# Kernel optimization log

Measured on AMD Instinct MI355X. Metric: run time of the kernel, lower is better.

Reference implementation:

```python
import jax, jax.numpy as jnp
import numpy as np

B = 8192
INPUT_DIM = 1024
HIDDEN = 4096
LATENT = 256
K = 16384  # codebook size
COMMIT = 0.25


def setup_inputs() -> dict:
    key = jax.random.key(0)
    ks = jax.random.split(key, 12)

    def lin(k, fan_in, fan_out):
        bound = 1.0 / np.sqrt(fan_in)
        kw, kb = jax.random.split(k)
        W = jax.random.uniform(kw, (fan_in, fan_out), jnp.float32, -bound, bound)
        b = jax.random.uniform(kb, (fan_out,), jnp.float32, -bound, bound)
        return W, b

    eW1, eb1 = lin(ks[0], INPUT_DIM, HIDDEN)
    eW2, eb2 = lin(ks[1], HIDDEN, HIDDEN)
    eW3, eb3 = lin(ks[2], HIDDEN, LATENT)
    dW1, db1 = lin(ks[3], LATENT, HIDDEN)
    dW2, db2 = lin(ks[4], HIDDEN, HIDDEN)
    dW3, db3 = lin(ks[5], HIDDEN, INPUT_DIM)
    codebook = jax.random.uniform(ks[6], (K, LATENT), jnp.float32, -1.0 / K, 1.0 / K)
    x = jax.random.normal(ks[7], (B, INPUT_DIM), jnp.float32)
    return {
        "x": x,
        "eW1": eW1, "eb1": eb1, "eW2": eW2, "eb2": eb2, "eW3": eW3, "eb3": eb3,
        "codebook": codebook,
        "dW1": dW1, "db1": db1, "dW2": dW2, "db2": db2, "dW3": dW3, "db3": db3,
    }


def _encoder(x, eW1, eb1, eW2, eb2, eW3, eb3):
    h = jax.nn.relu(x @ eW1 + eb1)          # dropout is identity in eval
    h = jax.nn.relu(h @ eW2 + eb2)
    return jnp.tanh(h @ eW3 + eb3)          # [B, LATENT]


def _decoder(z, dW1, db1, dW2, db2, dW3, db3):
    h = jax.nn.relu(z @ dW1 + db1)
    h = jax.nn.relu(h @ dW2 + db2)
    return h @ dW3 + db3                    # [B, INPUT_DIM]


def _vq(z, codebook):
    # pairwise squared distances: ||z||^2 + ||e||^2 - 2 z.e^T   -> [B, K]
    d = (jnp.sum(z * z, axis=1, keepdims=True)
         + jnp.sum(codebook * codebook, axis=1)
         - 2.0 * (z @ codebook.T))
    idx = jnp.argmin(d, axis=1)                              # [B]
    enc = jax.nn.one_hot(idx, K, dtype=jnp.float32)          # [B, K]
    q = enc @ codebook                                       # [B, LATENT]
    e_loss = jnp.mean((jax.lax.stop_gradient(q) - z) ** 2)
    q_loss = jnp.mean((q - jax.lax.stop_gradient(z)) ** 2)
    vq_loss = q_loss + COMMIT * e_loss
    q_st = z + jax.lax.stop_gradient(q - z)                  # straight-through
    avg_probs = jnp.mean(enc, axis=0)
    perplexity = jnp.exp(-jnp.sum(avg_probs * jnp.log(avg_probs + 1e-10)))
    return q_st, idx, vq_loss, perplexity


def reference(x, eW1, eb1, eW2, eb2, eW3, eb3, codebook,
              dW1, db1, dW2, db2, dW3, db3):
    z = _encoder(x, eW1, eb1, eW2, eb2, eW3, eb3)
    q, tokens, vq_loss, perplexity = _vq(z, codebook)
    recon = _decoder(q, dW1, db1, dW2, db2, dW3, db3)
    recon_loss = jnp.mean((recon - x) ** 2)
    total = vq_loss + recon_loss
    return recon, tokens, vq_loss, recon_loss, total, perplexity
```

## Files before the change

### kernel.cpp

```cpp
#include <hip/hip_runtime.h>
#include <stdint.h>

#define B_N 8192
#define D_IN 1024
#define D_HID 4096
#define D_LAT 256
#define K_CB 16384

typedef __attribute__((ext_vector_type(8))) short bf16x8;
typedef __attribute__((ext_vector_type(4))) float f32x4;

enum { EPI_RELU = 0, EPI_TANH = 1, EPI_RECON = 2, EPI_VQ = 3 };
enum { MEPI_RELU = 0, MEPI_RECON = 1 };

__device__ __forceinline__ unsigned short f2b(float v) {
  unsigned u = __float_as_uint(v);
  u += 0x7fffu + ((u >> 16) & 1u);
  return (unsigned short)(u >> 16);
}

template <int EPI, bool BT>
__global__ __launch_bounds__(256, 2) void gemm_k(
    const float* __restrict__ A, const float* __restrict__ Bm,
    const float* __restrict__ bias, float* __restrict__ C, int M, int N, int K,
    const float* __restrict__ zz, const float* __restrict__ ee,
    unsigned long long* __restrict__ keys, const float* __restrict__ xref,
    double* __restrict__ accums) {
  constexpr int BSTR = BT ? 132 : 128;
  __shared__ float As[16 * 260];
  __shared__ float Bs[16 * 132];
  const int tid = threadIdx.x;
  const int w = tid >> 6;
  const int tx = tid & 15, ty = tid >> 4;
  const int m0 = blockIdx.y << 8, n0 = blockIdx.x << 7;

  float acc[16][8];
#pragma unroll
  for (int i = 0; i < 16; ++i)
#pragma unroll
    for (int j = 0; j < 8; ++j) acc[i][j] = 0.0f;

  for (int k0 = 0; k0 < K; k0 += 16) {
#pragma unroll
    for (int r = 0; r < 4; ++r) {
      const int f = tid + (r << 8);
      const int m = f >> 2, kq = (f & 3) << 2;
      const float4 v = *(const float4*)(A + (size_t)(m0 + m) * K + k0 + kq);
      As[(kq + 0) * 260 + m] = v.x;
      As[(kq + 1) * 260 + m] = v.y;
      As[(kq + 2) * 260 + m] = v.z;
      As[(kq + 3) * 260 + m] = v.w;
    }
    if (!BT) {
#pragma unroll
      for (int r = 0; r < 2; ++r) {
        const int f = tid + (r << 8);
        const float* gp = Bm + (size_t)(k0 + (f >> 5)) * N + n0 + ((f & 31) << 2);
        __builtin_amdgcn_global_load_lds((const unsigned int*)gp,
                                         (unsigned int*)&Bs[(r << 10) + (w << 8)],
                                         16, 0, 0);
      }
    } else {
#pragma unroll
      for (int r = 0; r < 2; ++r) {
        const int f = tid + (r << 8);
        const int n = f >> 2, kq = (f & 3) << 2;
        const float4 v = *(const float4*)(Bm + (size_t)(n0 + n) * K + k0 + kq);
        Bs[(kq + 0) * BSTR + n] = v.x;
        Bs[(kq + 1) * BSTR + n] = v.y;
        Bs[(kq + 2) * BSTR + n] = v.z;
        Bs[(kq + 3) * BSTR + n] = v.w;
      }
    }
    __syncthreads();
#pragma unroll
    for (int kk = 0; kk < 16; ++kk) {
      float a[16], b[8];
#pragma unroll
      for (int q = 0; q < 4; ++q)
        *(float4*)(a + (q << 2)) = *(const float4*)(&As[kk * 260 + (q << 6) + (ty << 2)]);
      *(float4*)(b) = *(const float4*)(&Bs[kk * BSTR + (tx << 2)]);
      *(float4*)(b + 4) = *(const float4*)(&Bs[kk * BSTR + 64 + (tx << 2)]);
#pragma unroll
      for (int i = 0; i < 16; ++i)
#pragma unroll
        for (int j = 0; j < 8; ++j) acc[i][j] = fmaf(a[i], b[j], acc[i][j]);
    }
    __syncthreads();
  }

  if (EPI == EPI_VQ) {
    float zr[16];
#pragma unroll
    for (int i = 0; i < 16; ++i)
      zr[i] = zz[m0 + ((i >> 2) << 6) + (ty << 2) + (i & 3)];
    float ev[8];
    *(float4*)(ev) = *(const float4*)(ee + n0 + (tx << 2));
    *(float4*)(ev + 4) = *(const float4*)(ee + n0 + 64 + (tx << 2));
#pragma unroll
    for (int i = 0; i < 16; ++i) {
      unsigned long long bk = ~0ull;
#pragma unroll
      for (int j = 0; j < 8; ++j) {
        const int col = n0 + ((j >> 2) << 6) + (tx << 2) + (j & 3);
        const float t = zr[i] + ev[j];
        const float d = t - 2.0f * acc[i][j];
        unsigned u = __float_as_uint(d);
        u = (u & 0x80000000u) ? ~u : (u | 0x80000000u);
        const unsigned long long key = ((unsigned long long)u << 32) | (unsigned)col;
        bk = key < bk ? key : bk;
      }
#pragma unroll
      for (int s = 1; s <= 8; s <<= 1) {
        const unsigned long long o = __shfl_xor(bk, s);
        if (o < bk) bk = o;
      }
      if (tx == 0) {
        const int row = m0 + ((i >> 2) << 6) + (ty << 2) + (i & 3);
        atomicMin(keys + row, bk);
      }
    }
    return;
  }

  float bb[8];
  *(float4*)(bb) = *(const float4*)(bias + n0 + (tx << 2));
  *(float4*)(bb + 4) = *(const float4*)(bias + n0 + 64 + (tx << 2));
  double lsum = 0.0;
#pragma unroll
  for (int i = 0; i < 16; ++i) {
    const int row = m0 + ((i >> 2) << 6) + (ty << 2) + (i & 3);
    float vrow[8];
#pragma unroll
    for (int j = 0; j < 8; ++j) {
      float v = acc[i][j] + bb[j];
      if (EPI == EPI_RELU) v = fmaxf(v, 0.0f);
      if (EPI == EPI_TANH) v = tanhf(v);
      if (EPI == EPI_RECON) {
        const int col = n0 + ((j >> 2) << 6) + (tx << 2) + (j & 3);
        const float xr = xref[(size_t)row * N + col];
        const float df = v - xr;
        lsum += (double)df * (double)df;
      }
      vrow[j] = v;
    }
    *(float4*)(C + (size_t)row * N + n0 + (tx << 2)) = *(float4*)(vrow);
    *(float4*)(C + (size_t)row * N + n0 + 64 + (tx << 2)) = *(float4*)(vrow + 4);
  }
  if (EPI == EPI_RECON) {
#pragma unroll
    for (int o = 32; o; o >>= 1) lsum += __shfl_down(lsum, o);
    if ((tid & 63) == 0) atomicAdd(accums + 1, lsum);
  }
}

template <int EPI>
__global__ __launch_bounds__(256, 2) void gemm_s(
    const float* __restrict__ A, const float* __restrict__ Bm,
    const float* __restrict__ bias, float* __restrict__ C, int M, int N, int K) {
  __shared__ float As[16][128];
  __shared__ float Bs[16][128];
  const int tid = threadIdx.x;
  const int tx = tid & 15, ty = tid >> 4;
  const int m0 = blockIdx.y << 7, n0 = blockIdx.x << 7;
  float acc[8][8];
#pragma unroll
  for (int i = 0; i < 8; ++i)
#pragma unroll
    for (int j = 0; j < 8; ++j) acc[i][j] = 0.0f;
  for (int k0 = 0; k0 < K; k0 += 16) {
#pragma unroll
    for (int r = 0; r < 2; ++r) {
      const int f = tid + (r << 8);
      const int m = f >> 2, kq = (f & 3) << 2;
      const float4 v = *(const float4*)(A + (size_t)(m0 + m) * K + k0 + kq);
      As[kq + 0][m] = v.x; As[kq + 1][m] = v.y;
      As[kq + 2][m] = v.z; As[kq + 3][m] = v.w;
    }
#pragma unroll
    for (int r = 0; r < 2; ++r) {
      const int f = tid + (r << 8);
      const int k = f >> 5, nq = (f & 31) << 2;
      *(float4*)(&Bs[k][nq]) = *(const float4*)(Bm + (size_t)(k0 + k) * N + n0 + nq);
    }
    __syncthreads();
#pragma unroll
    for (int kk = 0; kk < 16; ++kk) {
      float a[8], b[8];
      *(float4*)(a) = *(const float4*)(&As[kk][ty << 2]);
      *(float4*)(a + 4) = *(const float4*)(&As[kk][64 + (ty << 2)]);
      *(float4*)(b) = *(const float4*)(&Bs[kk][tx << 2]);
      *(float4*)(b + 4) = *(const float4*)(&Bs[kk][64 + (tx << 2)]);
#pragma unroll
      for (int i = 0; i < 8; ++i)
#pragma unroll
        for (int j = 0; j < 8; ++j) acc[i][j] = fmaf(a[i], b[j], acc[i][j]);
    }
    __syncthreads();
  }
  float bb[8];
  *(float4*)(bb) = *(const float4*)(bias + n0 + (tx << 2));
  *(float4*)(bb + 4) = *(const float4*)(bias + n0 + 64 + (tx << 2));
#pragma unroll
  for (int i = 0; i < 8; ++i) {
    const int row = m0 + ((i < 4) ? (ty << 2) + i : 64 + (ty << 2) + i - 4);
    float vrow[8];
#pragma unroll
    for (int j = 0; j < 8; ++j) {
      float v = acc[i][j] + bb[j];
      if (EPI == EPI_RELU) v = fmaxf(v, 0.0f);
      if (EPI == EPI_TANH) v = tanhf(v);
      vrow[j] = v;
    }
    *(float4*)(C + (size_t)row * N + n0 + (tx << 2)) = *(float4*)(vrow);
    *(float4*)(C + (size_t)row * N + n0 + 64 + (tx << 2)) = *(float4*)(vrow + 4);
  }
}

template <int EPI>
__global__ __launch_bounds__(256, 2) void mgemm_k(
    const unsigned short* __restrict__ A, const unsigned short* __restrict__ Bt,
    const float* __restrict__ bias, void* __restrict__ Cout, int M, int N,
    int K, const float* __restrict__ xref, double* __restrict__ accums) {
  __shared__ __align__(16) unsigned short As[4096];
  __shared__ __align__(16) unsigned short Bs[4096];
  const int tid = threadIdx.x;
  const int w = tid >> 6, l = tid & 63;
  const int wr = w >> 1, wc = w & 1;
  const int g = l >> 4, tx = l & 15;
  const int m0 = blockIdx.y << 7, n0 = blockIdx.x << 7;

  f32x4 acc[4][4];
#pragma unroll
  for (int i = 0; i < 4; ++i)
#pragma unroll
    for (int j = 0; j < 4; ++j) acc[i][j] = (f32x4)0.0f;

  for (int k0 = 0; k0 < K; k0 += 32) {
#pragma unroll
    for (int c = 0; c < 2; ++c) {
      const int f = tid + (c << 8);
      const unsigned short* ga =
          A + (size_t)(m0 + (f >> 2)) * K + k0 + ((f & 3) << 3);
      __builtin_amdgcn_global_load_lds((const unsigned int*)ga,
                                       (unsigned int*)&As[(c << 11) + (w << 9)],
                                       16, 0, 0);
      const unsigned short* gb =
          Bt + (size_t)(n0 + (f >> 2)) * K + k0 + ((f & 3) << 3);
      __builtin_amdgcn_global_load_lds((const unsigned int*)gb,
                                       (unsigned int*)&Bs[(c << 11) + (w << 9)],
                                       16, 0, 0);
    }
    __syncthreads();
    bf16x8 af[4], bfv[4];
#pragma unroll
    for (int f = 0; f < 4; ++f) {
      af[f] = *(const bf16x8*)&As[((wr << 6) + (f << 4) + tx) * 32 + (g << 3)];
      bfv[f] = *(const bf16x8*)&Bs[((wc << 6) + (f << 4) + tx) * 32 + (g << 3)];
    }
#pragma unroll
    for (int fm = 0; fm < 4; ++fm)
#pragma unroll
      for (int fn = 0; fn < 4; ++fn)
        acc[fm][fn] = __builtin_amdgcn_mfma_f32_16x16x32_bf16(
            af[fm], bfv[fn], acc[fm][fn], 0, 0, 0);
    __syncthreads();
  }

  double lsum = 0.0;
#pragma unroll
  for (int fm = 0; fm < 4; ++fm) {
    const int row0 = m0 + (wr << 6) + (fm << 4) + (g << 2);
#pragma unroll
    for (int fn = 0; fn < 4; ++fn) {
      const int col = n0 + (wc << 6) + (fn << 4) + tx;
      const float bb = bias[col];
#pragma unroll
      for (int r = 0; r < 4; ++r) {
        float v = acc[fm][fn][r] + bb;
        if (EPI == MEPI_RELU) {
          v = fmaxf(v, 0.0f);
          ((unsigned short*)Cout)[(size_t)(row0 + r) * N + col] = f2b(v);
        } else {
          const float xr = xref[(size_t)(row0 + r) * N + col];
          const float df = v - xr;
          lsum += (double)df * (double)df;
          ((float*)Cout)[(size_t)(row0 + r) * N + col] = v;
        }
      }
    }
  }
  if (EPI == MEPI_RECON) {
#pragma unroll
    for (int o = 32; o; o >>= 1) lsum += __shfl_down(lsum, o);
    if (l == 0) atomicAdd(accums + 1, lsum);
  }
}

__global__ void castT_k(const float* __restrict__ W,
                        unsigned short* __restrict__ out, int K, int N) {
  __shared__ float t[32][33];
  const int tx = threadIdx.x & 31, ty4 = threadIdx.x >> 5;
  const int nb = blockIdx.x << 5, kb = blockIdx.y << 5;
#pragma unroll
  for (int r = 0; r < 4; ++r) {
    const int k = (ty4 << 2) + r;
    t[k][tx] = W[(size_t)(kb + k) * N + nb + tx];
  }
  __syncthreads();
#pragma unroll
  for (int r = 0; r < 4; ++r) {
    const int n = (ty4 << 2) + r;
    out[(size_t)(nb + n) * K + kb + tx] = f2b(t[tx][n]);
  }
}

__global__ void rowsumsq(const float* __restrict__ v, float* __restrict__ out,
                         int rows) {
  const int w = (int)((blockIdx.x * blockDim.x + threadIdx.x) >> 6);
  const int lane = threadIdx.x & 63;
  if (w >= rows) return;
  const float4 x = *(const float4*)(v + (size_t)w * 256 + (lane << 2));
  float s = ((x.x * x.x + x.y * x.y) + x.z * x.z) + x.w * x.w;
#pragma unroll
  for (int o = 32; o; o >>= 1) s += __shfl_down(s, o);
  if (lane == 0) out[w] = s;
}

__global__ void finalize_vq(const unsigned long long* __restrict__ keys,
                            const float* __restrict__ z,
                            const float* __restrict__ cb,
                            unsigned short* __restrict__ qst_bf,
                            float* __restrict__ tok, int* __restrict__ counts,
                            double* __restrict__ accums) {
  const int row = (int)((blockIdx.x * blockDim.x + threadIdx.x) >> 6);
  const int lane = threadIdx.x & 63;
  if (row >= B_N) return;
  const int idx = (int)(keys[row] & 0xffffffffull);
  const float4 zv = *(const float4*)(z + (size_t)row * 256 + (lane << 2));
  const float4 evv = *(const float4*)(cb + (size_t)idx * 256 + (lane << 2));
  float4 q;
  double s = 0.0;
  float d;
  d = evv.x - zv.x; q.x = zv.x + d; s += (double)d * (double)d;
  d = evv.y - zv.y; q.y = zv.y + d; s += (double)d * (double)d;
  d = evv.z - zv.z; q.z = zv.z + d; s += (double)d * (double)d;
  d = evv.w - zv.w; q.w = zv.w + d; s += (double)d * (double)d;
  ushort4 qb;
  qb.x = f2b(q.x); qb.y = f2b(q.y); qb.z = f2b(q.z); qb.w = f2b(q.w);
  *(ushort4*)(qst_bf + (size_t)row * 256 + (lane << 2)) = qb;
#pragma unroll
  for (int o = 32; o; o >>= 1) s += __shfl_down(s, o);
  if (lane == 0) {
    atomicAdd(accums + 0, s);
    tok[row] = (float)idx;
    atomicAdd(counts + idx, 1);
  }
}

__global__ void finalize_scalars(const int* __restrict__ counts,
                                 const double* __restrict__ accums,
                                 float* __restrict__ outs) {
  __shared__ double red[256];
  double h = 0.0;
  for (int k = threadIdx.x; k < K_CB; k += 256) {
    const float p = (float)counts[k] * (1.0f / 8192.0f);
    const float t = p * logf(p + 1e-10f);
    h += (double)t;
  }
  red[threadIdx.x] = h;
  __syncthreads();
  for (int s = 128; s; s >>= 1) {
    if ((int)threadIdx.x < s) red[threadIdx.x] += red[threadIdx.x + s];
    __syncthreads();
  }
  if (threadIdx.x == 0) {
    const float perp = expf((float)(-red[0]));
    const float m1 = (float)(accums[0] * (1.0 / ((double)B_N * (double)D_LAT)));
    const float vq = m1 + 0.25f * m1;
    const float rl = (float)(accums[1] * (1.0 / ((double)B_N * (double)D_IN)));
    outs[0] = vq;
    outs[1] = rl;
    outs[2] = vq + rl;
    outs[3] = perp;
  }
}

extern "C" void kernel_launch(void* const* d_in, const int* in_sizes, int n_in,
                              void* d_out, int out_size, void* d_ws,
                              size_t ws_size, hipStream_t stream) {
  (void)in_sizes; (void)n_in; (void)out_size;
  const float* x   = (const float*)d_in[0];
  const float* eW1 = (const float*)d_in[1];
  const float* eb1 = (const float*)d_in[2];
  const float* eW2 = (const float*)d_in[3];
  const float* eb2 = (const float*)d_in[4];
  const float* eW3 = (const float*)d_in[5];
  const float* eb3 = (const float*)d_in[6];
  const float* cb  = (const float*)d_in[7];
  const float* dW1 = (const float*)d_in[8];
  const float* db1 = (const float*)d_in[9];
  const float* dW2 = (const float*)d_in[10];
  const float* db2 = (const float*)d_in[11];
  const float* dW3 = (const float*)d_in[12];
  const float* db3 = (const float*)d_in[13];
  float* out = (float*)d_out;

  char* ws = (char*)d_ws;
  const size_t OFF_Z      = 0;
  const size_t OFF_EEV    = OFF_Z + (size_t)B_N * D_LAT * 4;
  const size_t OFF_ZZV    = OFF_EEV + (size_t)K_CB * 4;
  const size_t OFF_KEYS   = OFF_ZZV + (size_t)B_N * 4;
  const size_t OFF_COUNTS = OFF_KEYS + (size_t)B_N * 8;
  const size_t OFF_ACC    = OFF_COUNTS + (size_t)K_CB * 4;
  const size_t OFF_QB     = OFF_ACC + 256;
  const size_t OFF_H      = OFF_QB + (size_t)B_N * D_LAT * 2;

  float* z    = (float*)(ws + OFF_Z);
  float* eev  = (float*)(ws + OFF_EEV);
  float* zzv  = (float*)(ws + OFF_ZZV);
  unsigned long long* keys = (unsigned long long*)(ws + OFF_KEYS);
  int* counts = (int*)(ws + OFF_COUNTS);
  double* accums = (double*)(ws + OFF_ACC);
  unsigned short* qst_bf = (unsigned short*)(ws + OFF_QB);

  int c_enc = 256;
  for (int c = 8192; c >= 256; c >>= 1)
    if (OFF_H + 2ull * c * D_HID * 4 <= ws_size) { c_enc = c; break; }
  float* hA = (float*)(ws + OFF_H);
  float* hB = hA + (size_t)c_enc * D_HID;

  const size_t SZ_WB1 = (size_t)D_HID * D_LAT * 2;
  const size_t SZ_WB2 = (size_t)D_HID * D_HID * 2;
  const size_t SZ_WB3 = (size_t)D_IN * D_HID * 2;
  const size_t OFF_DECH = OFF_H + SZ_WB1 + SZ_WB2 + SZ_WB3;
  int c_dec = 128;
  for (int c = 8192; c >= 128; c >>= 1)
    if (OFF_DECH + 2ull * c * D_HID * 2 <= ws_size) { c_dec = c; break; }
  unsigned short* wB1 = (unsigned short*)(ws + OFF_H);
  unsigned short* wB2 = (unsigned short*)(ws + OFF_H + SZ_WB1);
  unsigned short* wB3 = (unsigned short*)(ws + OFF_H + SZ_WB1 + SZ_WB2);
  unsigned short* hbfA = (unsigned short*)(ws + OFF_DECH);
  unsigned short* hbfB = hbfA + (size_t)c_dec * D_HID;

  float* tok_out = out + (size_t)B_N * D_IN;
  float* scal_out = tok_out + B_N;

  hipMemsetAsync(keys, 0xFF, (size_t)B_N * 8, stream);
  hipMemsetAsync(counts, 0, (size_t)K_CB * 4, stream);
  hipMemsetAsync(accums, 0, 2 * sizeof(double), stream);

  rowsumsq<<<(K_CB * 64) / 256, 256, 0, stream>>>(cb, eev, K_CB);

  const bool big = (c_enc >= 4096);
  for (int c0 = 0; c0 < B_N; c0 += c_enc) {
    if (big) {
      const dim3 gH(D_HID / 128, c_enc / 256);
      gemm_k<EPI_RELU, false><<<gH, 256, 0, stream>>>(
          x + (size_t)c0 * D_IN, eW1, eb1, hA, c_enc, D_HID, D_IN,
          nullptr, nullptr, nullptr, nullptr, nullptr);
      gemm_k<EPI_RELU, false><<<gH, 256, 0, stream>>>(
          hA, eW2, eb2, hB, c_enc, D_HID, D_HID,
          nullptr, nullptr, nullptr, nullptr, nullptr);
    } else {
      const dim3 gH(D_HID / 128, c_enc / 128);
      gemm_s<EPI_RELU><<<gH, 256, 0, stream>>>(
          x + (size_t)c0 * D_IN, eW1, eb1, hA, c_enc, D_HID, D_IN);
      gemm_s<EPI_RELU><<<gH, 256, 0, stream>>>(
          hA, eW2, eb2, hB, c_enc, D_HID, D_HID);
    }
    gemm_s<EPI_TANH><<<dim3(D_LAT / 128, c_enc / 128), 256, 0, stream>>>(
        hB, eW3, eb3, z + (size_t)c0 * D_LAT, c_enc, D_LAT, D_HID);
  }

  rowsumsq<<<(B_N * 64) / 256, 256, 0, stream>>>(z, zzv, B_N);

  gemm_k<EPI_VQ, true><<<dim3(K_CB / 128, B_N / 256), 256, 0, stream>>>(
      z, cb, nullptr, nullptr, B_N, K_CB, D_LAT, zzv, eev, keys, nullptr,
      nullptr);
  finalize_vq<<<(B_N * 64) / 256, 256, 0, stream>>>(keys, z, cb, qst_bf,
                                                    tok_out, counts, accums);

  castT_k<<<dim3(D_HID / 32, D_LAT / 32), 256, 0, stream>>>(dW1, wB1, D_LAT, D_HID);
  castT_k<<<dim3(D_HID / 32, D_HID / 32), 256, 0, stream>>>(dW2, wB2, D_HID, D_HID);
  castT_k<<<dim3(D_IN / 32, D_HID / 32), 256, 0, stream>>>(dW3, wB3, D_HID, D_IN);

  for (int c0 = 0; c0 < B_N; c0 += c_dec) {
    const dim3 gH(D_HID / 128, c_dec / 128);
    mgemm_k<MEPI_RELU><<<gH, 256, 0, stream>>>(
        qst_bf + (size_t)c0 * D_LAT, wB1, db1, hbfA, c_dec, D_HID, D_LAT,
        nullptr, nullptr);
    mgemm_k<MEPI_RELU><<<gH, 256, 0, stream>>>(
        hbfA, wB2, db2, hbfB, c_dec, D_HID, D_HID, nullptr, nullptr);
    mgemm_k<MEPI_RECON><<<dim3(D_IN / 128, c_dec / 128), 256, 0, stream>>>(
        hbfB, wB3, db3, out + (size_t)c0 * D_IN, c_dec, D_IN, D_HID,
        x + (size_t)c0 * D_IN, accums);
  }

  finalize_scalars<<<1, 256, 0, stream>>>(counts, accums, scal_out);
}
```

Measured before the change: 6.420 ms.

## Split-K the latent encoder GEMM, retile VQ, and swizzle big-GEMM blocks

The final encoder layer (N=256) now runs as a 4-way split-K GEMM that writes partial sums into the free hidden buffer, followed by a combine kernel that adds bias and applies tanh. This raises the block count of a narrow GEMM that previously had very few blocks. The VQ distance GEMM moves to a 128x128 tile with its own transposed codebook load, the big encoder GEMM gets an XCD-aware block-index remap, and the templated kernels are split into dedicated ones. The cost is extra partial-sum traffic plus one more kernel launch per chunk.

```diff
diff --git a/kernel.cpp b/kernel.cpp
--- a/kernel.cpp
+++ b/kernel.cpp
@@ -10,29 +10,31 @@
 typedef __attribute__((ext_vector_type(8))) short bf16x8;
 typedef __attribute__((ext_vector_type(4))) float f32x4;
 
-enum { EPI_RELU = 0, EPI_TANH = 1, EPI_RECON = 2, EPI_VQ = 3 };
-enum { MEPI_RELU = 0, MEPI_RECON = 1 };
-
 __device__ __forceinline__ unsigned short f2b(float v) {
   unsigned u = __float_as_uint(v);
   u += 0x7fffu + ((u >> 16) & 1u);
   return (unsigned short)(u >> 16);
 }
 
-template <int EPI, bool BT>
-__global__ __launch_bounds__(256, 2) void gemm_k(
+__global__ __launch_bounds__(256, 2) void enc_big_k(
     const float* __restrict__ A, const float* __restrict__ Bm,
-    const float* __restrict__ bias, float* __restrict__ C, int M, int N, int K,
-    const float* __restrict__ zz, const float* __restrict__ ee,
-    unsigned long long* __restrict__ keys, const float* __restrict__ xref,
-    double* __restrict__ accums) {
-  constexpr int BSTR = BT ? 132 : 128;
+    const float* __restrict__ bias, float* __restrict__ C, int M, int N,
+    int K) {
   __shared__ float As[16 * 260];
-  __shared__ float Bs[16 * 132];
+  __shared__ float Bs[16 * 128];
   const int tid = threadIdx.x;
   const int w = tid >> 6;
   const int tx = tid & 15, ty = tid >> 4;
-  const int m0 = blockIdx.y << 8, n0 = blockIdx.x << 7;
+  int bx = blockIdx.x, by = blockIdx.y;
+  {
+    const int gx = gridDim.x, n = gx * gridDim.y;
+    const int wg = by * gx + bx;
+    const int q = n >> 3;
+    const int s = (wg & 7) * q + (wg >> 3);
+    bx = s % gx;
+    by = s / gx;
+  }
+  const int m0 = by << 8, n0 = bx << 7;
 
   float acc[16][8];
 #pragma unroll
@@ -51,26 +53,13 @@
       As[(kq + 2) * 260 + m] = v.z;
       As[(kq + 3) * 260 + m] = v.w;
     }
-    if (!BT) {
-#pragma unroll
-      for (int r = 0; r < 2; ++r) {
-        const int f = tid + (r << 8);
-        const float* gp = Bm + (size_t)(k0 + (f >> 5)) * N + n0 + ((f & 31) << 2);
-        __builtin_amdgcn_global_load_lds((const unsigned int*)gp,
-                                         (unsigned int*)&Bs[(r << 10) + (w << 8)],
-                                         16, 0, 0);
-      }
-    } else {
-#pragma unroll
-      for (int r = 0; r < 2; ++r) {
-        const int f = tid + (r << 8);
-        const int n = f >> 2, kq = (f & 3) << 2;
-        const float4 v = *(const float4*)(Bm + (size_t)(n0 + n) * K + k0 + kq);
-        Bs[(kq + 0) * BSTR + n] = v.x;
-        Bs[(kq + 1) * BSTR + n] = v.y;
-        Bs[(kq + 2) * BSTR + n] = v.z;
-        Bs[(kq + 3) * BSTR + n] = v.w;
-      }
+#pragma unroll
+    for (int r = 0; r < 2; ++r) {
+      const int f = tid + (r << 8);
+      const float* gp = Bm + (size_t)(k0 + (f >> 5)) * N + n0 + ((f & 31) << 2);
+      __builtin_amdgcn_global_load_lds((const unsigned int*)gp,
+                                       (unsigned int*)&Bs[(r << 10) + (w << 8)],
+                                       16, 0, 0);
     }
     __syncthreads();
 #pragma unroll
@@ -78,86 +67,36 @@
       float a[16], b[8];
 #pragma unroll
       for (int q = 0; q < 4; ++q)
-        *(float4*)(a + (q << 2)) = *(const float4*)(&As[kk * 260 + (q << 6) + (ty << 2)]);
-      *(float4*)(b) = *(const float4*)(&Bs[kk * BSTR + (tx << 2)]);
-      *(float4*)(b + 4) = *(const float4*)(&Bs[kk * BSTR + 64 + (tx << 2)]);
+        *(float4*)(a + (q << 2)) =
+            *(const float4*)(&As[kk * 260 + (q << 6) + (ty << 2)]);
+      *(float4*)(b) = *(const float4*)(&Bs[kk * 128 + (tx << 2)]);
+      *(float4*)(b + 4) = *(const float4*)(&Bs[kk * 128 + 64 + (tx << 2)]);
 #pragma unroll
       for (int i = 0; i < 16; ++i)
 #pragma unroll
         for (int j = 0; j < 8; ++j) acc[i][j] = fmaf(a[i], b[j], acc[i][j]);
     }
     __syncthreads();
-  }
-
-  if (EPI == EPI_VQ) {
-    float zr[16];
-#pragma unroll
-    for (int i = 0; i < 16; ++i)
-      zr[i] = zz[m0 + ((i >> 2) << 6) + (ty << 2) + (i & 3)];
-    float ev[8];
-    *(float4*)(ev) = *(const float4*)(ee + n0 + (tx << 2));
-    *(float4*)(ev + 4) = *(const float4*)(ee + n0 + 64 + (tx << 2));
-#pragma unroll
-    for (int i = 0; i < 16; ++i) {
-      unsigned long long bk = ~0ull;
-#pragma unroll
-      for (int j = 0; j < 8; ++j) {
-        const int col = n0 + ((j >> 2) << 6) + (tx << 2) + (j & 3);
-        const float t = zr[i] + ev[j];
-        const float d = t - 2.0f * acc[i][j];
-        unsigned u = __float_as_uint(d);
-        u = (u & 0x80000000u) ? ~u : (u | 0x80000000u);
-        const unsigned long long key = ((unsigned long long)u << 32) | (unsigned)col;
-        bk = key < bk ? key : bk;
-      }
-#pragma unroll
-      for (int s = 1; s <= 8; s <<= 1) {
-        const unsigned long long o = __shfl_xor(bk, s);
-        if (o < bk) bk = o;
-      }
-      if (tx == 0) {
-        const int row = m0 + ((i >> 2) << 6) + (ty << 2) + (i & 3);
-        atomicMin(keys + row, bk);
-      }
-    }
-    return;
   }
 
   float bb[8];
   *(float4*)(bb) = *(const float4*)(bias + n0 + (tx << 2));
   *(float4*)(bb + 4) = *(const float4*)(bias + n0 + 64 + (tx << 2));
-  double lsum = 0.0;
 #pragma unroll
   for (int i = 0; i < 16; ++i) {
     const int row = m0 + ((i >> 2) << 6) + (ty << 2) + (i & 3);
     float vrow[8];
 #pragma unroll
-    for (int j = 0; j < 8; ++j) {
-      float v = acc[i][j] + bb[j];
-      if (EPI == EPI_RELU) v = fmaxf(v, 0.0f);
-      if (EPI == EPI_TANH) v = tanhf(v);
-      if (EPI == EPI_RECON) {
-        const int col = n0 + ((j >> 2) << 6) + (tx << 2) + (j & 3);
-        const float xr = xref[(size_t)row * N + col];
-        const float df = v - xr;
-        lsum += (double)df * (double)df;
-      }
-      vrow[j] = v;
-    }
+    for (int j = 0; j < 8; ++j) vrow[j] = fmaxf(acc[i][j] + bb[j], 0.0f);
     *(float4*)(C + (size_t)row * N + n0 + (tx << 2)) = *(float4*)(vrow);
     *(float4*)(C + (size_t)row * N + n0 + 64 + (tx << 2)) = *(float4*)(vrow + 4);
   }
-  if (EPI == EPI_RECON) {
-#pragma unroll
-    for (int o = 32; o; o >>= 1) lsum += __shfl_down(lsum, o);
-    if ((tid & 63) == 0) atomicAdd(accums + 1, lsum);
-  }
-}
-
-template <int EPI>
-__global__ __launch_bounds__(256, 2) void gemm_s(
+}
+
+__global__ __launch_bounds__(256, 2) void enc_small_k(
     const float* __restrict__ A, const float* __restrict__ Bm,
-    const float* __restrict__ bias, float* __restrict__ C, int M, int N, int K) {
+    const float* __restrict__ bias, float* __restrict__ C, int M, int N,
+    int K) {
   __shared__ float As[16][128];
   __shared__ float Bs[16][128];
   const int tid = threadIdx.x;
@@ -181,7 +120,8 @@
     for (int r = 0; r < 2; ++r) {
       const int f = tid + (r << 8);
       const int k = f >> 5, nq = (f & 31) << 2;
-      *(float4*)(&Bs[k][nq]) = *(const float4*)(Bm + (size_t)(k0 + k) * N + n0 + nq);
+      *(float4*)(&Bs[k][nq]) =
+          *(const float4*)(Bm + (size_t)(k0 + k) * N + n0 + nq);
     }
     __syncthreads();
 #pragma unroll
@@ -206,19 +146,170 @@
     const int row = m0 + ((i < 4) ? (ty << 2) + i : 64 + (ty << 2) + i - 4);
     float vrow[8];
 #pragma unroll
-    for (int j = 0; j < 8; ++j) {
-      float v = acc[i][j] + bb[j];
-      if (EPI == EPI_RELU) v = fmaxf(v, 0.0f);
-      if (EPI == EPI_TANH) v = tanhf(v);
-      vrow[j] = v;
-    }
+    for (int j = 0; j < 8; ++j) vrow[j] = fmaxf(acc[i][j] + bb[j], 0.0f);
     *(float4*)(C + (size_t)row * N + n0 + (tx << 2)) = *(float4*)(vrow);
     *(float4*)(C + (size_t)row * N + n0 + 64 + (tx << 2)) = *(float4*)(vrow + 4);
   }
 }
 
+__global__ __launch_bounds__(256, 2) void enc3_part_k(
+    const float* __restrict__ A, const float* __restrict__ B,
+    float* __restrict__ P, int M, int K) {
+  __shared__ float As[16][128];
+  __shared__ float Bs[16][128];
+  const int tid = threadIdx.x;
+  const int tx = tid & 15, ty = tid >> 4;
+  const int m0 = blockIdx.y << 7, n0 = blockIdx.x << 7;
+  const int s = blockIdx.z;
+  const int kbeg = s * (K >> 2), kend = kbeg + (K >> 2);
+  float acc[8][8];
+#pragma unroll
+  for (int i = 0; i < 8; ++i)
+#pragma unroll
+    for (int j = 0; j < 8; ++j) acc[i][j] = 0.0f;
+  for (int k0 = kbeg; k0 < kend; k0 += 16) {
+#pragma unroll
+    for (int r = 0; r < 2; ++r) {
+      const int f = tid + (r << 8);
+      const int m = f >> 2, kq = (f & 3) << 2;
+      const float4 v = *(const float4*)(A + (size_t)(m0 + m) * K + k0 + kq);
+      As[kq + 0][m] = v.x; As[kq + 1][m] = v.y;
+      As[kq + 2][m] = v.z; As[kq + 3][m] = v.w;
+    }
+#pragma unroll
+    for (int r = 0; r < 2; ++r) {
+      const int f = tid + (r << 8);
+      const int k = f >> 5, nq = (f & 31) << 2;
+      *(float4*)(&Bs[k][nq]) =
+          *(const float4*)(B + (size_t)(k0 + k) * D_LAT + n0 + nq);
+    }
+    __syncthreads();
+#pragma unroll
+    for (int kk = 0; kk < 16; ++kk) {
+      float a[8], b[8];
+      *(float4*)(a) = *(const float4*)(&As[kk][ty << 2]);
+      *(float4*)(a + 4) = *(const float4*)(&As[kk][64 + (ty << 2)]);
+      *(float4*)(b) = *(const float4*)(&Bs[kk][tx << 2]);
+      *(float4*)(b + 4) = *(const float4*)(&Bs[kk][64 + (tx << 2)]);
+#pragma unroll
+      for (int i = 0; i < 8; ++i)
+#pragma unroll
+        for (int j = 0; j < 8; ++j) acc[i][j] = fmaf(a[i], b[j], acc[i][j]);
+    }
+    __syncthreads();
+  }
+  float* Ps = P + (size_t)s * M * D_LAT;
+#pragma unroll
+  for (int i = 0; i < 8; ++i) {
+    const int row = m0 + ((i < 4) ? (ty << 2) + i : 64 + (ty << 2) + i - 4);
+    *(float4*)(Ps + (size_t)row * D_LAT + n0 + (tx << 2)) = *(float4*)(&acc[i][0]);
+    *(float4*)(Ps + (size_t)row * D_LAT + n0 + 64 + (tx << 2)) = *(float4*)(&acc[i][4]);
+  }
+}
+
+__global__ void enc3_comb_k(const float* __restrict__ P,
+                            const float* __restrict__ bias,
+                            float* __restrict__ z, int M) {
+  const size_t i4 = (size_t)blockIdx.x * blockDim.x + threadIdx.x;
+  const size_t tot = (size_t)M * (D_LAT / 4);
+  if (i4 >= tot) return;
+  const size_t sstr = (size_t)M * (D_LAT / 4);
+  const float4* Pv = (const float4*)P;
+  float4 v = Pv[i4];
+  const float4 v1 = Pv[i4 + sstr];
+  const float4 v2 = Pv[i4 + 2 * sstr];
+  const float4 v3 = Pv[i4 + 3 * sstr];
+  const int col = (int)((i4 << 2) & (D_LAT - 1));
+  const float4 bb = *(const float4*)(bias + col);
+  float4 o;
+  o.x = tanhf(((v.x + v1.x) + v2.x) + v3.x + bb.x);
+  o.y = tanhf(((v.y + v1.y) + v2.y) + v3.y + bb.y);
+  o.z = tanhf(((v.z + v1.z) + v2.z) + v3.z + bb.z);
+  o.w = tanhf(((v.w + v1.w) + v2.w) + v3.w + bb.w);
+  ((float4*)z)[i4] = o;
+}
+
+__global__ __launch_bounds__(256, 2) void vq_k(
+    const float* __restrict__ A, const float* __restrict__ Bm,
+    const float* __restrict__ zz, const float* __restrict__ ee,
+    unsigned long long* __restrict__ keys) {
+  __shared__ float As[16][128];
+  __shared__ float Bs[16][128];
+  const int tid = threadIdx.x;
+  const int tx = tid & 15, ty = tid >> 4;
+  const int m0 = blockIdx.y << 7, n0 = blockIdx.x << 7;
+  const int K = D_LAT;
+  float acc[8][8];
+#pragma unroll
+  for (int i = 0; i < 8; ++i)
+#pragma unroll
+    for (int j = 0; j < 8; ++j) acc[i][j] = 0.0f;
+  for (int k0 = 0; k0 < K; k0 += 16) {
+#pragma unroll
+    for (int r = 0; r < 2; ++r) {
+      const int f = tid + (r << 8);
+      const int m = f >> 2, kq = (f & 3) << 2;
+      const float4 v = *(const float4*)(A + (size_t)(m0 + m) * K + k0 + kq);
+      As[kq + 0][m] = v.x; As[kq + 1][m] = v.y;
+      As[kq + 2][m] = v.z; As[kq + 3][m] = v.w;
+    }
+#pragma unroll
+    for (int r = 0; r < 2; ++r) {
+      const int f = tid + (r << 8);
+      const int n = f >> 2, kq = (f & 3) << 2;
+      const float4 v = *(const float4*)(Bm + (size_t)(n0 + n) * K + k0 + kq);
+      Bs[kq + 0][n] = v.x; Bs[kq + 1][n] = v.y;
+      Bs[kq + 2][n] = v.z; Bs[kq + 3][n] = v.w;
+    }
+    __syncthreads();
+#pragma unroll
+    for (int kk = 0; kk < 16; ++kk) {
+      float a[8], b[8];
+      *(float4*)(a) = *(const float4*)(&As[kk][ty << 2]);
+      *(float4*)(a + 4) = *(const float4*)(&As[kk][64 + (ty << 2)]);
+      *(float4*)(b) = *(const float4*)(&Bs[kk][tx << 2]);
+      *(float4*)(b + 4) = *(const float4*)(&Bs[kk][64 + (tx << 2)]);
+#pragma unroll
+      for (int i = 0; i < 8; ++i)
+#pragma unroll
+        for (int j = 0; j < 8; ++j) acc[i][j] = fmaf(a[i], b[j], acc[i][j]);
+    }
+    __syncthreads();
+  }
+  float zr[8];
+#pragma unroll
+  for (int i = 0; i < 8; ++i)
+    zr[i] = zz[m0 + ((i < 4) ? (ty << 2) + i : 64 + (ty << 2) + i - 4)];
+  float ev[8];
+  *(float4*)(ev) = *(const float4*)(ee + n0 + (tx << 2));
+  *(float4*)(ev + 4) = *(const float4*)(ee + n0 + 64 + (tx << 2));
+#pragma unroll
+  for (int i = 0; i < 8; ++i) {
+    unsigned long long bk = ~0ull;
+#pragma unroll
+    for (int j = 0; j < 8; ++j) {
+      const int col = n0 + ((j < 4) ? (tx << 2) + j : 64 + (tx << 2) + j - 4);
+      const float t = zr[i] + ev[j];
+      const float d = t - 2.0f * acc[i][j];
+      unsigned u = __float_as_uint(d);
+      u = (u & 0x80000000u) ? ~u : (u | 0x80000000u);
+      const unsigned long long key = ((unsigned long long)u << 32) | (unsigned)col;
+      bk = key < bk ? key : bk;
+    }
+#pragma unroll
+    for (int s = 1; s <= 8; s <<= 1) {
+      const unsigned long long o = __shfl_xor(bk, s);
+      if (o < bk) bk = o;
+    }
+    if (tx == 0) {
+      const int row = m0 + ((i < 4) ? (ty << 2) + i : 64 + (ty << 2) + i - 4);
+      atomicMin(keys + row, bk);
+    }
+  }
+}
+
 template <int EPI>
-__global__ __launch_bounds__(256, 2) void mgemm_k(
+__device__ __forceinline__ void mgemm_body(
     const unsigned short* __restrict__ A, const unsigned short* __restrict__ Bt,
     const float* __restrict__ bias, void* __restrict__ Cout, int M, int N,
     int K, const float* __restrict__ xref, double* __restrict__ accums) {
@@ -278,7 +369,7 @@
 #pragma unroll
       for (int r = 0; r < 4; ++r) {
         float v = acc[fm][fn][r] + bb;
-        if (EPI == MEPI_RELU) {
+        if (EPI == 0) {
           v = fmaxf(v, 0.0f);
           ((unsigned short*)Cout)[(size_t)(row0 + r) * N + col] = f2b(v);
         } else {
@@ -290,11 +381,22 @@
       }
     }
   }
-  if (EPI == MEPI_RECON) {
+  if (EPI == 1) {
 #pragma unroll
     for (int o = 32; o; o >>= 1) lsum += __shfl_down(lsum, o);
     if (l == 0) atomicAdd(accums + 1, lsum);
   }
+}
+
+__global__ __launch_bounds__(256, 2) void dec_relu_k(
+    const unsigned short* A, const unsigned short* Bt, const float* bias,
+    unsigned short* Cout, int M, int N, int K) {
+  mgemm_body<0>(A, Bt, bias, Cout, M, N, K, nullptr, nullptr);
+}
+__global__ __launch_bounds__(256, 2) void dec_recon_k(
+    const unsigned short* A, const unsigned short* Bt, const float* bias,
+    float* Cout, int M, int N, int K, const float* xref, double* accums) {
+  mgemm_body<1>(A, Bt, bias, Cout, M, N, K, xref, accums);
 }
 
 __global__ void castT_k(const float* __restrict__ W,
@@ -429,6 +531,7 @@
     if (OFF_H + 2ull * c * D_HID * 4 <= ws_size) { c_enc = c; break; }
   float* hA = (float*)(ws + OFF_H);
   float* hB = hA + (size_t)c_enc * D_HID;
+  float* P3 = hA;
 
   const size_t SZ_WB1 = (size_t)D_HID * D_LAT * 2;
   const size_t SZ_WB2 = (size_t)D_HID * D_HID * 2;
@@ -456,28 +559,25 @@
   for (int c0 = 0; c0 < B_N; c0 += c_enc) {
     if (big) {
       const dim3 gH(D_HID / 128, c_enc / 256);
-      gemm_k<EPI_RELU, false><<<gH, 256, 0, stream>>>(
-          x + (size_t)c0 * D_IN, eW1, eb1, hA, c_enc, D_HID, D_IN,
-          nullptr, nullptr, nullptr, nullptr, nullptr);
-      gemm_k<EPI_RELU, false><<<gH, 256, 0, stream>>>(
-          hA, eW2, eb2, hB, c_enc, D_HID, D_HID,
-          nullptr, nullptr, nullptr, nullptr, nullptr);
+      enc_big_k<<<gH, 256, 0, stream>>>(x + (size_t)c0 * D_IN, eW1, eb1, hA,
+                                        c_enc, D_HID, D_IN);
+      enc_big_k<<<gH, 256, 0, stream>>>(hA, eW2, eb2, hB, c_enc, D_HID, D_HID);
     } else {
       const dim3 gH(D_HID / 128, c_enc / 128);
-      gemm_s<EPI_RELU><<<gH, 256, 0, stream>>>(
-          x + (size_t)c0 * D_IN, eW1, eb1, hA, c_enc, D_HID, D_IN);
-      gemm_s<EPI_RELU><<<gH, 256, 0, stream>>>(
-          hA, eW2, eb2, hB, c_enc, D_HID, D_HID);
-    }
-    gemm_s<EPI_TANH><<<dim3(D_LAT / 128, c_enc / 128), 256, 0, stream>>>(
-        hB, eW3, eb3, z + (size_t)c0 * D_LAT, c_enc, D_LAT, D_HID);
+      enc_small_k<<<gH, 256, 0, stream>>>(x + (size_t)c0 * D_IN, eW1, eb1, hA,
+                                          c_enc, D_HID, D_IN);
+      enc_small_k<<<gH, 256, 0, stream>>>(hA, eW2, eb2, hB, c_enc, D_HID,
+                                          D_HID);
+    }
+    enc3_part_k<<<dim3(D_LAT / 128, c_enc / 128, 4), 256, 0, stream>>>(
+        hB, eW3, P3, c_enc, D_HID);
+    enc3_comb_k<<<(c_enc * (D_LAT / 4) + 255) / 256, 256, 0, stream>>>(
+        P3, eb3, z + (size_t)c0 * D_LAT, c_enc);
   }
 
   rowsumsq<<<(B_N * 64) / 256, 256, 0, stream>>>(z, zzv, B_N);
 
-  gemm_k<EPI_VQ, true><<<dim3(K_CB / 128, B_N / 256), 256, 0, stream>>>(
-      z, cb, nullptr, nullptr, B_N, K_CB, D_LAT, zzv, eev, keys, nullptr,
-      nullptr);
+  vq_k<<<dim3(K_CB / 128, B_N / 128), 256, 0, stream>>>(z, cb, zzv, eev, keys);
   finalize_vq<<<(B_N * 64) / 256, 256, 0, stream>>>(keys, z, cb, qst_bf,
                                                     tok_out, counts, accums);
 
@@ -487,12 +587,11 @@
 
   for (int c0 = 0; c0 < B_N; c0 += c_dec) {
     const dim3 gH(D_HID / 128, c_dec / 128);
-    mgemm_k<MEPI_RELU><<<gH, 256, 0, stream>>>(
-        qst_bf + (size_t)c0 * D_LAT, wB1, db1, hbfA, c_dec, D_HID, D_LAT,
-        nullptr, nullptr);
-    mgemm_k<MEPI_RELU><<<gH, 256, 0, stream>>>(
-        hbfA, wB2, db2, hbfB, c_dec, D_HID, D_HID, nullptr, nullptr);
-    mgemm_k<MEPI_RECON><<<dim3(D_IN / 128, c_dec / 128), 256, 0, stream>>>(
+    dec_relu_k<<<gH, 256, 0, stream>>>(qst_bf + (size_t)c0 * D_LAT, wB1, db1,
+                                       hbfA, c_dec, D_HID, D_LAT);
+    dec_relu_k<<<gH, 256, 0, stream>>>(hbfA, wB2, db2, hbfB, c_dec, D_HID,
+                                       D_HID);
+    dec_recon_k<<<dim3(D_IN / 128, c_dec / 128), 256, 0, stream>>>(
         hbfB, wB3, db3, out + (size_t)c0 * D_IN, c_dec, D_IN, D_HID,
         x + (size_t)c0 * D_IN, accums);
   }
```

After: 5.612 ms. 1.14x faster.
